# Optimization experiments

Hardware: AMD Instinct MI355X
Metric: run time of the kernel (lower is better)

Reference implementation:

```python
import jax, jax.numpy as jnp
import numpy as np

N_SIDE = 64            # regular RBF kernel grid: 64^3 kernels
LC0_DIM = 32
CMIN, CMAX = -1.0, 1.0
COMBS = [(0, 1), (0, 2), (1, 2)]
# 2^3 cell-corner offsets for the 8 nearest regular-grid kernels
OFFS = np.array([[i, j, k] for i in (0, 1) for j in (0, 1) for k in (0, 1)], dtype=np.int32)


def grid_sample_2d(plane, coords):
    """Bilinear, align_corners=True. plane [C,H,W]; coords [N,2] in [-1,1];
    coords[:,0] indexes W, coords[:,1] indexes H (torch grid_sample convention)."""
    C, H, W = plane.shape
    x = (coords[:, 0] + 1.0) * 0.5 * (W - 1)
    y = (coords[:, 1] + 1.0) * 0.5 * (H - 1)
    x0 = jnp.clip(jnp.floor(x), 0, W - 2).astype(jnp.int32)
    y0 = jnp.clip(jnp.floor(y), 0, H - 2).astype(jnp.int32)
    wx = (x - x0)[None, :]
    wy = (y - y0)[None, :]
    p00 = plane[:, y0, x0]
    p01 = plane[:, y0, x0 + 1]
    p10 = plane[:, y0 + 1, x0]
    p11 = plane[:, y0 + 1, x0 + 1]
    out = p00 * (1 - wx) * (1 - wy) + p01 * wx * (1 - wy) + p10 * (1 - wx) * wy + p11 * wx * wy
    return out.T  # [N,C]


def rbf_features(x, lc0, ks):
    """Regular-grid kNN (8 cell corners) + inverse-quadratic RBF weighting of local codes."""
    interval = (CMAX - CMIN) / (N_SIDE - 1)
    cell = jnp.clip(jnp.floor((x - CMIN) / interval), 0, N_SIDE - 2).astype(jnp.int32)  # [N,3]
    corner = cell[:, None, :] + jnp.asarray(OFFS)[None]                                  # [N,8,3]
    idx = (corner[..., 0] * N_SIDE + corner[..., 1]) * N_SIDE + corner[..., 2]           # [N,8]
    kc = CMIN + corner.astype(x.dtype) * interval                                        # [N,8,3] kernel centers
    d2 = jnp.sum((x[:, None, :] - kc) ** 2, axis=-1)                                     # [N,8]
    s = ks[idx]                                                                          # [N,8] per-kernel shape
    phi = 1.0 / (1.0 + d2 * s * s)                                                       # ivq RBF
    phi = phi / (jnp.sum(phi, axis=-1, keepdims=True) + 1e-8)                            # rbf_lc0_normalize
    codes = lc0[idx]                                                                     # [N,8,LC0_DIM]
    return jnp.einsum('nk,nkd->nd', phi, codes)


def setup_inputs() -> dict:
    key = jax.random.key(0)
    ks_ = jax.random.split(key, 16)
    N = 524288
    aabb = jnp.array([[-1.5, -1.5, -1.5], [1.5, 1.5, 1.5]], dtype=jnp.float32)
    pts = jax.random.uniform(ks_[0], (N, 3), minval=-1.5, maxval=1.5, dtype=jnp.float32)

    def plane(k, r):  # kp_init uniform(0.1, 0.5)
        return jax.random.uniform(k, (32, r, r), minval=0.1, maxval=0.5, dtype=jnp.float32)

    resos = [128, 256, 512]
    inp = {'pts': pts, 'aabb': aabb}
    ki = 1
    for si, r in enumerate(resos):
        for ci in range(3):
            inp[f'p{si}{ci}'] = plane(ks_[ki], r)
            ki += 1
    inp['lc0'] = jax.random.uniform(ks_[ki], (N_SIDE ** 3, LC0_DIM), minval=-1e-4, maxval=1e-4, dtype=jnp.float32)
    interval = (CMAX - CMIN) / (N_SIDE - 1)
    inp['ks'] = jnp.full((N_SIDE ** 3,), 1.0 / interval, dtype=jnp.float32)  # ks_alpha=1.0
    inp['kpb'] = jax.random.uniform(ks_[ki + 1], (96 + LC0_DIM,), minval=-1e-4, maxval=1e-4, dtype=jnp.float32)
    return inp


def reference(pts, aabb, p00, p01, p02, p10, p11, p12, p20, p21, p22, lc0, ks, kpb):
    planes = [[p00, p01, p02], [p10, p11, p12], [p20, p21, p22]]
    # normalize_aabb -> [-1,1]
    x = (pts - aabb[0]) * (2.0 / (aabb[1] - aabb[0])) - 1.0
    # interpolate_ms_features: product over planes within a scale, concat across scales
    feats = []
    for scale in planes:
        interp = 1.0
        for pl, comb in zip(scale, COMBS):
            interp = interp * grid_sample_2d(pl, x[:, list(comb)])
        feats.append(interp)
    kp = jnp.concatenate(feats, axis=-1)          # [N,96]
    rbf = rbf_features(x, lc0, ks)                # [N,32]
    return jnp.concatenate([kp, rbf], axis=-1) + kpb  # [N,128], + kpb bias
```

## Files before the change

### kernel.cpp

```cpp
#include <hip/hip_runtime.h>
#include <hip/hip_bf16.h>
#include <stdint.h>

typedef __hip_bfloat16 bf16;
typedef __hip_bfloat162 bf162;

#define S0 ((size_t)(128*128*32))
#define S1 ((size_t)(256*256*32))
#define S2 ((size_t)(512*512*32))
#define LCN ((size_t)(64*64*64*32))

#define T128 (128*128/64)
#define T256 (256*256/64)
#define T512 (512*512/64)
#define TPLANES (3*T128 + 3*T256 + 3*T512)
#define TLC2 ((int)(LCN/2048))

#define NBUCKETS 32768

__device__ __forceinline__ uint32_t mpart(uint32_t x)
{
    x = (x | (x << 16)) & 0x030000FFu;
    x = (x | (x << 8))  & 0x0300F00Fu;
    x = (x | (x << 4))  & 0x030C30C3u;
    x = (x | (x << 2))  & 0x09249249u;
    return x;
}

__device__ __forceinline__ uint32_t bucket_of(float xn, float yn, float zn)
{
    float bx = fminf(fmaxf(floorf((xn + 1.0f) * 16.0f), 0.0f), 31.0f);
    float by = fminf(fmaxf(floorf((yn + 1.0f) * 16.0f), 0.0f), 31.0f);
    float bz = fminf(fmaxf(floorf((zn + 1.0f) * 16.0f), 0.0f), 31.0f);
    return mpart((uint32_t)bx) | (mpart((uint32_t)by) << 1) | (mpart((uint32_t)bz) << 2);
}

__device__ __forceinline__ uint32_t pack2(float a, float b)
{
    union { bf162 h; uint32_t u; } cv;
    cv.h = __halves2bfloat162(__float2bfloat16(a), __float2bfloat16(b));
    return cv.u;
}

__device__ __forceinline__ void unpack8(uint4 u, float* f)
{
    const bf162* h = (const bf162*)&u;
    f[0] = __bfloat162float(h[0].x); f[1] = __bfloat162float(h[0].y);
    f[2] = __bfloat162float(h[1].x); f[3] = __bfloat162float(h[1].y);
    f[4] = __bfloat162float(h[2].x); f[5] = __bfloat162float(h[2].y);
    f[6] = __bfloat162float(h[3].x); f[7] = __bfloat162float(h[3].y);
}

__global__ __launch_bounds__(256) void zero_counts_kernel(unsigned int* __restrict__ counts)
{
    counts[blockIdx.x * 256 + threadIdx.x] = 0u;
}

__global__ __launch_bounds__(256) void transpose_kernel(
    const float* __restrict__ p00, const float* __restrict__ p01, const float* __restrict__ p02,
    const float* __restrict__ p10, const float* __restrict__ p11, const float* __restrict__ p12,
    const float* __restrict__ p20, const float* __restrict__ p21, const float* __restrict__ p22,
    bf16* __restrict__ tp0, bf16* __restrict__ tp1, bf16* __restrict__ tp2)
{
    const int b = blockIdx.x;
    const int tid = threadIdx.x;
    __shared__ float t[64 * 33];
    const float* src; bf16* dst; int HW, tile;
    if (b < 3 * T128) {
        int pid = b >> 8; tile = b & (T128 - 1); HW = 128 * 128;
        src = pid == 0 ? p00 : (pid == 1 ? p01 : p02);
        dst = tp0 + (size_t)pid * S0;
    } else if (b < 3 * T128 + 3 * T256) {
        int bb = b - 3 * T128; int pid = bb >> 10; tile = bb & (T256 - 1); HW = 256 * 256;
        src = pid == 0 ? p10 : (pid == 1 ? p11 : p12);
        dst = tp1 + (size_t)pid * S1;
    } else {
        int bb = b - 3 * T128 - 3 * T256; int pid = bb >> 12; tile = bb & (T512 - 1); HW = 512 * 512;
        src = pid == 0 ? p20 : (pid == 1 ? p21 : p22);
        dst = tp2 + (size_t)pid * S2;
    }
    const int base = tile * 64;
#pragma unroll
    for (int i = 0; i < 2; ++i) {
        int linear = i * 256 + tid;
        int ch = linear >> 4, pq = linear & 15;
        float4 v = *(const float4*)(src + (size_t)ch * HW + base + pq * 4);
        t[(pq * 4 + 0) * 33 + ch] = v.x;
        t[(pq * 4 + 1) * 33 + ch] = v.y;
        t[(pq * 4 + 2) * 33 + ch] = v.z;
        t[(pq * 4 + 3) * 33 + ch] = v.w;
    }
    __syncthreads();
    {
        int pos = tid >> 2, chunk = tid & 3;
        const float* row = t + pos * 33 + chunk * 8;
        uint4 o;
        o.x = pack2(row[0], row[1]);
        o.y = pack2(row[2], row[3]);
        o.z = pack2(row[4], row[5]);
        o.w = pack2(row[6], row[7]);
        *(uint4*)(dst + (size_t)(base + pos) * 32 + chunk * 8) = o;
    }
}

__global__ __launch_bounds__(256) void lc0cast_kernel(
    const float* __restrict__ lc0, bf16* __restrict__ lc0b)
{
    size_t off = (size_t)blockIdx.x * 2048 + (size_t)threadIdx.x * 8;
    float4 v0 = *(const float4*)(lc0 + off);
    float4 v1 = *(const float4*)(lc0 + off + 4);
    uint4 o;
    o.x = pack2(v0.x, v0.y);
    o.y = pack2(v0.z, v0.w);
    o.z = pack2(v1.x, v1.y);
    o.w = pack2(v1.z, v1.w);
    *(uint4*)(lc0b + off) = o;
}

__global__ __launch_bounds__(256) void hist_kernel(
    const float* __restrict__ pts, const float* __restrict__ aabb,
    unsigned int* __restrict__ counts, int N)
{
    int g = blockIdx.x * 256 + threadIdx.x;
    int b0 = g * 4;
    if (b0 >= N) return;
    float a0 = aabb[0], a1 = aabb[1], a2 = aabb[2];
    float sx = 2.0f / (aabb[3] - a0);
    float sy = 2.0f / (aabb[4] - a1);
    float sz = 2.0f / (aabb[5] - a2);
    if (b0 + 3 < N) {
        const float4* p4 = (const float4*)(pts + (size_t)b0 * 3);
        float4 A = p4[0], B = p4[1], C = p4[2];
        float px[4] = {A.x, A.w, B.z, C.y};
        float py[4] = {A.y, B.x, B.w, C.z};
        float pz[4] = {A.z, B.y, C.x, C.w};
#pragma unroll
        for (int k = 0; k < 4; ++k) {
            float xn = (px[k] - a0) * sx - 1.0f;
            float yn = (py[k] - a1) * sy - 1.0f;
            float zn = (pz[k] - a2) * sz - 1.0f;
            atomicAdd(&counts[bucket_of(xn, yn, zn)], 1u);
        }
    } else {
        for (int i = b0; i < N; ++i) {
            float xn = (pts[3 * (size_t)i + 0] - a0) * sx - 1.0f;
            float yn = (pts[3 * (size_t)i + 1] - a1) * sy - 1.0f;
            float zn = (pts[3 * (size_t)i + 2] - a2) * sz - 1.0f;
            atomicAdd(&counts[bucket_of(xn, yn, zn)], 1u);
        }
    }
}

__global__ __launch_bounds__(1024) void scan_kernel(unsigned int* __restrict__ counts)
{
    __shared__ unsigned int sums[1024];
    const int t = threadIdx.x;
    unsigned int local[32];
    unsigned int s = 0;
#pragma unroll
    for (int i = 0; i < 32; ++i) { local[i] = counts[t * 32 + i]; s += local[i]; }
    sums[t] = s;
    __syncthreads();
    for (int off = 1; off < 1024; off <<= 1) {
        unsigned int v = (t >= off) ? sums[t - off] : 0u;
        __syncthreads();
        sums[t] += v;
        __syncthreads();
    }
    unsigned int run = sums[t] - s;
#pragma unroll
    for (int i = 0; i < 32; ++i) { unsigned int c = local[i]; counts[t * 32 + i] = run; run += c; }
}

__global__ __launch_bounds__(256) void scatter_kernel(
    const float* __restrict__ pts, const float* __restrict__ aabb,
    unsigned int* __restrict__ offsets, float4* __restrict__ sp, int N)
{
    int g = blockIdx.x * 256 + threadIdx.x;
    int b0 = g * 4;
    if (b0 >= N) return;
    float a0 = aabb[0], a1 = aabb[1], a2 = aabb[2];
    float sx = 2.0f / (aabb[3] - a0);
    float sy = 2.0f / (aabb[4] - a1);
    float sz = 2.0f / (aabb[5] - a2);
    if (b0 + 3 < N) {
        const float4* p4 = (const float4*)(pts + (size_t)b0 * 3);
        float4 A = p4[0], B = p4[1], C = p4[2];
        float px[4] = {A.x, A.w, B.z, C.y};
        float py[4] = {A.y, B.x, B.w, C.z};
        float pz[4] = {A.z, B.y, C.x, C.w};
#pragma unroll
        for (int k = 0; k < 4; ++k) {
            float xn = (px[k] - a0) * sx - 1.0f;
            float yn = (py[k] - a1) * sy - 1.0f;
            float zn = (pz[k] - a2) * sz - 1.0f;
            unsigned int pos = atomicAdd(&offsets[bucket_of(xn, yn, zn)], 1u);
            float4 v; v.x = xn; v.y = yn; v.z = zn; v.w = __int_as_float(b0 + k);
            sp[pos] = v;
        }
    } else {
        for (int i = b0; i < N; ++i) {
            float xn = (pts[3 * (size_t)i + 0] - a0) * sx - 1.0f;
            float yn = (pts[3 * (size_t)i + 1] - a1) * sy - 1.0f;
            float zn = (pts[3 * (size_t)i + 2] - a2) * sz - 1.0f;
            unsigned int pos = atomicAdd(&offsets[bucket_of(xn, yn, zn)], 1u);
            float4 v; v.x = xn; v.y = yn; v.z = zn; v.w = __int_as_float(i);
            sp[pos] = v;
        }
    }
}

template <int R>
__device__ __forceinline__ void sample_tp16(const uint4* __restrict__ tq,
                                            float cx, float cy, int cq, float* o)
{
    float gx = (cx + 1.0f) * (0.5f * (float)(R - 1));
    float gy = (cy + 1.0f) * (0.5f * (float)(R - 1));
    float fx = fminf(fmaxf(floorf(gx), 0.0f), (float)(R - 2));
    float fy = fminf(fmaxf(floorf(gy), 0.0f), (float)(R - 2));
    float wx = gx - fx, wy = gy - fy;
    int ix = (int)fx, iy = (int)fy;
    int t00 = (iy * R + ix) * 4 + cq;
    uint4 u00 = tq[t00];
    uint4 u01 = tq[t00 + 4];
    uint4 u10 = tq[t00 + R * 4];
    uint4 u11 = tq[t00 + R * 4 + 4];
    float w11 = wx * wy;
    float w01 = wx - w11;
    float w10 = wy - w11;
    float w00 = 1.0f - wx - wy + w11;
    float a[8], b[8], c[8], d[8];
    unpack8(u00, a); unpack8(u01, b); unpack8(u10, c); unpack8(u11, d);
#pragma unroll
    for (int j = 0; j < 8; ++j)
        o[j] = a[j] * w00 + b[j] * w01 + c[j] * w10 + d[j] * w11;
}

template <int R>
__device__ __forceinline__ void plane_feat16(const uint4* __restrict__ tq,
                                             float xn, float yn, float zn, int cq, float* acc)
{
    const int ps = R * R * 4;
    float t0[8];
    sample_tp16<R>(tq,          xn, yn, cq, acc);
    sample_tp16<R>(tq + ps,     xn, zn, cq, t0);
#pragma unroll
    for (int j = 0; j < 8; ++j) acc[j] *= t0[j];
    sample_tp16<R>(tq + 2 * ps, yn, zn, cq, t0);
#pragma unroll
    for (int j = 0; j < 8; ++j) acc[j] *= t0[j];
}

__device__ __forceinline__ void rbf16(const uint4* __restrict__ lcq,
                                      const float* __restrict__ ks,
                                      float xn, float yn, float zn, int cq, float* acc)
{
    const float interval = 2.0f / 63.0f;
    const float invi = 31.5f;
    float fc0 = fminf(fmaxf(floorf((xn + 1.0f) * invi), 0.0f), 62.0f);
    float fc1 = fminf(fmaxf(floorf((yn + 1.0f) * invi), 0.0f), 62.0f);
    float fc2 = fminf(fmaxf(floorf((zn + 1.0f) * invi), 0.0f), 62.0f);
    int c0 = (int)fc0, c1 = (int)fc1, c2 = (int)fc2;
    float dx0 = xn - (-1.0f + fc0 * interval), dx1 = dx0 - interval;
    float dy0 = yn - (-1.0f + fc1 * interval), dy1 = dy0 - interval;
    float dz0 = zn - (-1.0f + fc2 * interval), dz1 = dz0 - interval;
    int ibase = (c0 * 64 + c1) * 64 + c2;

    float phi[8]; int id[8];
    float sum = 0.0f;
#pragma unroll
    for (int k = 0; k < 8; ++k) {
        int i = (k >> 2) & 1, j = (k >> 1) & 1, l = k & 1;
        int idx = ibase + i * 4096 + j * 64 + l;
        id[k] = idx;
        float ddx = i ? dx1 : dx0;
        float ddy = j ? dy1 : dy0;
        float ddz = l ? dz1 : dz0;
        float dd = ddx * ddx + ddy * ddy + ddz * ddz;
        float s = ks[idx];
        float ph = __builtin_amdgcn_rcpf(fmaf(dd, s * s, 1.0f));
        phi[k] = ph;
        sum += ph;
    }
    float inv = __builtin_amdgcn_rcpf(sum + 1e-8f);
#pragma unroll
    for (int j = 0; j < 8; ++j) acc[j] = 0.0f;
#pragma unroll
    for (int k = 0; k < 8; ++k) {
        float w = phi[k] * inv;
        uint4 u = lcq[id[k] * 4 + cq];
        float v[8]; unpack8(u, v);
#pragma unroll
        for (int j = 0; j < 8; ++j) acc[j] = fmaf(w, v[j], acc[j]);
    }
}

__global__ __launch_bounds__(256) void field16_kernel(
    const uint4* __restrict__ tq0, const uint4* __restrict__ tq1, const uint4* __restrict__ tq2,
    const uint4* __restrict__ lcq,
    const float* __restrict__ ks, const float* __restrict__ kpb,
    const float4* __restrict__ sp, float* __restrict__ out, int N)
{
    const int wave = threadIdx.x >> 6;
    const int lane = threadIdx.x & 63;
    const int p    = lane >> 2;
    const int cq   = lane & 3;
    int bid = blockIdx.x;
    int nb = gridDim.x;
    if ((nb & 7) == 0) bid = (bid & 7) * (nb >> 3) + (bid >> 3);
    const int m = bid * 16 + p;
    if (m >= N) return;

    float4 q = sp[m];
    float xn = q.x, yn = q.y, zn = q.z;
    int n = __float_as_int(q.w);

    float acc[8];
    int base;
    if (wave == 0)      { base = 0;  plane_feat16<128>(tq0, xn, yn, zn, cq, acc); }
    else if (wave == 1) { base = 32; plane_feat16<256>(tq1, xn, yn, zn, cq, acc); }
    else if (wave == 2) { base = 64; plane_feat16<512>(tq2, xn, yn, zn, cq, acc); }
    else                { base = 96; rbf16(lcq, ks, xn, yn, zn, cq, acc); }

    const float* kb = kpb + base + cq * 8;
    float4 k0 = *(const float4*)kb;
    float4 k1 = *(const float4*)(kb + 4);
    float* o = out + (size_t)n * 128 + base + cq * 8;
    float4 r0; r0.x = acc[0] + k0.x; r0.y = acc[1] + k0.y; r0.z = acc[2] + k0.z; r0.w = acc[3] + k0.w;
    float4 r1; r1.x = acc[4] + k1.x; r1.y = acc[5] + k1.y; r1.z = acc[6] + k1.z; r1.w = acc[7] + k1.w;
    *(float4*)o = r0;
    *(float4*)(o + 4) = r1;
}

template <int R>
__device__ __forceinline__ float2 sample_tp(const bf162* __restrict__ tp,
                                            float cx, float cy, int cpair)
{
    float gx = (cx + 1.0f) * (0.5f * (float)(R - 1));
    float gy = (cy + 1.0f) * (0.5f * (float)(R - 1));
    float fx = fminf(fmaxf(floorf(gx), 0.0f), (float)(R - 2));
    float fy = fminf(fmaxf(floorf(gy), 0.0f), (float)(R - 2));
    float wx = gx - fx, wy = gy - fy;
    int ix = (int)fx, iy = (int)fy;
    int i00 = (iy * R + ix) * 16 + cpair;
    int i10 = i00 + R * 16;
    bf162 v00 = tp[i00];
    bf162 v01 = tp[i00 + 16];
    bf162 v10 = tp[i10];
    bf162 v11 = tp[i10 + 16];
    float w11 = wx * wy;
    float w01 = wx - w11;
    float w10 = wy - w11;
    float w00 = 1.0f - wx - wy + w11;
    float2 r;
    r.x = __bfloat162float(v00.x) * w00 + __bfloat162float(v01.x) * w01
        + __bfloat162float(v10.x) * w10 + __bfloat162float(v11.x) * w11;
    r.y = __bfloat162float(v00.y) * w00 + __bfloat162float(v01.y) * w01
        + __bfloat162float(v10.y) * w10 + __bfloat162float(v11.y) * w11;
    return r;
}

template <int R>
__device__ __forceinline__ float2 plane_feat(const bf162* __restrict__ tp,
                                             float xn, float yn, float zn, int cpair)
{
    const int ps = R * R * 16;
    float2 a = sample_tp<R>(tp,          xn, yn, cpair);
    float2 b = sample_tp<R>(tp + ps,     xn, zn, cpair);
    float2 c = sample_tp<R>(tp + 2 * ps, yn, zn, cpair);
    float2 r; r.x = a.x * b.x * c.x; r.y = a.y * b.y * c.y;
    return r;
}

__device__ __forceinline__ float2 sample_f32(const float* __restrict__ pl, int R,
                                             float cx, float cy, int ch)
{
    float gx = (cx + 1.0f) * 0.5f * (float)(R - 1);
    float gy = (cy + 1.0f) * 0.5f * (float)(R - 1);
    float fx = fminf(fmaxf(floorf(gx), 0.0f), (float)(R - 2));
    float fy = fminf(fmaxf(floorf(gy), 0.0f), (float)(R - 2));
    float wx = gx - fx, wy = gy - fy;
    int ix = (int)fx, iy = (int)fy;
    float w11 = wx * wy, w01 = wx - w11, w10 = wy - w11, w00 = 1.0f - wx - wy + w11;
    size_t HW = (size_t)R * R;
    const float* q0 = pl + (size_t)ch * HW + (size_t)iy * R + ix;
    const float* q1 = q0 + HW;
    float2 r;
    r.x = q0[0] * w00 + q0[1] * w01 + q0[R] * w10 + q0[R + 1] * w11;
    r.y = q1[0] * w00 + q1[1] * w01 + q1[R] * w10 + q1[R + 1] * w11;
    return r;
}

template <bool TP>
__device__ __forceinline__ float2 rbf_feat(const bf162* __restrict__ lc0b,
                                           const float* __restrict__ lc0f,
                                           const float* __restrict__ ks,
                                           float xn, float yn, float zn, int cpair)
{
    const float interval = 2.0f / 63.0f;
    const float invi = 31.5f;
    float fc0 = fminf(fmaxf(floorf((xn + 1.0f) * invi), 0.0f), 62.0f);
    float fc1 = fminf(fmaxf(floorf((yn + 1.0f) * invi), 0.0f), 62.0f);
    float fc2 = fminf(fmaxf(floorf((zn + 1.0f) * invi), 0.0f), 62.0f);
    int c0 = (int)fc0, c1 = (int)fc1, c2 = (int)fc2;
    float dx0 = xn - (-1.0f + fc0 * interval), dx1 = dx0 - interval;
    float dy0 = yn - (-1.0f + fc1 * interval), dy1 = dy0 - interval;
    float dz0 = zn - (-1.0f + fc2 * interval), dz1 = dz0 - interval;
    int ibase = (c0 * 64 + c1) * 64 + c2;

    float phi[8]; int id[8];
    float sum = 0.0f;
#pragma unroll
    for (int k = 0; k < 8; ++k) {
        int i = (k >> 2) & 1, j = (k >> 1) & 1, l = k & 1;
        int idx = ibase + i * 4096 + j * 64 + l;
        id[k] = idx;
        float ddx = i ? dx1 : dx0;
        float ddy = j ? dy1 : dy0;
        float ddz = l ? dz1 : dz0;
        float dd = ddx * ddx + ddy * ddy + ddz * ddz;
        float s = ks[idx];
        float ph = __builtin_amdgcn_rcpf(fmaf(dd, s * s, 1.0f));
        phi[k] = ph;
        sum += ph;
    }
    float inv = __builtin_amdgcn_rcpf(sum + 1e-8f);
    float ax = 0.0f, ay = 0.0f;
#pragma unroll
    for (int k = 0; k < 8; ++k) {
        float w = phi[k] * inv;
        float vx, vy;
        if (TP) {
            bf162 v = lc0b[id[k] * 16 + cpair];
            vx = __bfloat162float(v.x); vy = __bfloat162float(v.y);
        } else {
            const float* cp = lc0f + (size_t)id[k] * 32 + 2 * cpair;
            vx = cp[0]; vy = cp[1];
        }
        ax = fmaf(w, vx, ax);
        ay = fmaf(w, vy, ay);
    }
    float2 r; r.x = ax; r.y = ay;
    return r;
}

template <bool TP>
__global__ __launch_bounds__(256) void field_legacy_kernel(
    const float* __restrict__ pts, const float* __restrict__ aabb,
    const float* __restrict__ p00, const float* __restrict__ p01, const float* __restrict__ p02,
    const float* __restrict__ p10, const float* __restrict__ p11, const float* __restrict__ p12,
    const float* __restrict__ p20, const float* __restrict__ p21, const float* __restrict__ p22,
    const bf162* __restrict__ tp0, const bf162* __restrict__ tp1, const bf162* __restrict__ tp2,
    const bf162* __restrict__ lc0b, const float* __restrict__ lc0f,
    const float* __restrict__ ks, const float* __restrict__ kpb,
    float* __restrict__ out, int N)
{
    const int wave  = threadIdx.x >> 6;
    const int lane  = threadIdx.x & 63;
    const int p     = lane >> 4;
    const int cpair = lane & 15;
    const int n = blockIdx.x * 4 + p;
    if (n >= N) return;

    float px = pts[3 * (size_t)n + 0];
    float py = pts[3 * (size_t)n + 1];
    float pz = pts[3 * (size_t)n + 2];
    float xn = (px - aabb[0]) * (2.0f / (aabb[3] - aabb[0])) - 1.0f;
    float yn = (py - aabb[1]) * (2.0f / (aabb[4] - aabb[1])) - 1.0f;
    float zn = (pz - aabb[2]) * (2.0f / (aabb[5] - aabb[2])) - 1.0f;

    float2 val;
    int f;
    if (wave == 0) {
        if (TP) val = plane_feat<128>(tp0, xn, yn, zn, cpair);
        else {
            float2 a = sample_f32(p00, 128, xn, yn, 2 * cpair);
            float2 b = sample_f32(p01, 128, xn, zn, 2 * cpair);
            float2 c = sample_f32(p02, 128, yn, zn, 2 * cpair);
            val.x = a.x * b.x * c.x; val.y = a.y * b.y * c.y;
        }
        f = 2 * cpair;
    } else if (wave == 1) {
        if (TP) val = plane_feat<256>(tp1, xn, yn, zn, cpair);
        else {
            float2 a = sample_f32(p10, 256, xn, yn, 2 * cpair);
            float2 b = sample_f32(p11, 256, xn, zn, 2 * cpair);
            float2 c = sample_f32(p12, 256, yn, zn, 2 * cpair);
            val.x = a.x * b.x * c.x; val.y = a.y * b.y * c.y;
        }
        f = 32 + 2 * cpair;
    } else if (wave == 2) {
        if (TP) val = plane_feat<512>(tp2, xn, yn, zn, cpair);
        else {
            float2 a = sample_f32(p20, 512, xn, yn, 2 * cpair);
            float2 b = sample_f32(p21, 512, xn, zn, 2 * cpair);
            float2 c = sample_f32(p22, 512, yn, zn, 2 * cpair);
            val.x = a.x * b.x * c.x; val.y = a.y * b.y * c.y;
        }
        f = 64 + 2 * cpair;
    } else {
        val = rbf_feat<TP>(lc0b, lc0f, ks, xn, yn, zn, cpair);
        f = 96 + 2 * cpair;
    }

    val.x += kpb[f];
    val.y += kpb[f + 1];
    *(float2*)(out + (size_t)n * 128 + f) = val;
}

extern "C" void kernel_launch(void* const* d_in, const int* in_sizes, int n_in,
                              void* d_out, int out_size, void* d_ws, size_t ws_size,
                              hipStream_t stream)
{
    const float* pts  = (const float*)d_in[0];
    const float* aabb = (const float*)d_in[1];
    const float* pl[9];
    for (int i = 0; i < 9; ++i) pl[i] = (const float*)d_in[2 + i];
    const float* lc0 = (const float*)d_in[11];
    const float* ks  = (const float*)d_in[12];
    const float* kpb = (const float*)d_in[13];
    float* out = (float*)d_out;
    const int N = in_sizes[0] / 3;

    const size_t needTP = (3 * (S0 + S1 + S2) + LCN) * sizeof(bf16);
    const size_t cntOff = needTP;
    const size_t spOff  = cntOff + (size_t)NBUCKETS * 4;
    const size_t needSort = spOff + (size_t)N * 16;

    bf16* w    = (bf16*)d_ws;
    bf16* tp0  = w;
    bf16* tp1  = tp0 + 3 * S0;
    bf16* tp2  = tp1 + 3 * S1;
    bf16* lc0b = tp2 + 3 * S2;
    unsigned int* counts = (unsigned int*)((char*)d_ws + cntOff);
    float4* sp = (float4*)((char*)d_ws + spOff);

    const bool useTP   = (d_ws != nullptr) && (ws_size >= needTP);
    const bool useSort = (d_ws != nullptr) && (ws_size >= needSort);

    if (useSort) {
        const int g4 = (N + 1023) / 1024;
        zero_counts_kernel<<<NBUCKETS / 256, 256, 0, stream>>>(counts);
        hist_kernel<<<g4, 256, 0, stream>>>(pts, aabb, counts, N);
        transpose_kernel<<<TPLANES, 256, 0, stream>>>(
            pl[0], pl[1], pl[2], pl[3], pl[4], pl[5], pl[6], pl[7], pl[8],
            tp0, tp1, tp2);
        lc0cast_kernel<<<TLC2, 256, 0, stream>>>(lc0, lc0b);
        scan_kernel<<<1, 1024, 0, stream>>>(counts);
        scatter_kernel<<<g4, 256, 0, stream>>>(pts, aabb, counts, sp, N);
        const int blocks16 = (N + 15) / 16;
        field16_kernel<<<blocks16, 256, 0, stream>>>(
            (const uint4*)tp0, (const uint4*)tp1, (const uint4*)tp2,
            (const uint4*)lc0b, ks, kpb, sp, out, N);
    } else if (useTP) {
        transpose_kernel<<<TPLANES, 256, 0, stream>>>(
            pl[0], pl[1], pl[2], pl[3], pl[4], pl[5], pl[6], pl[7], pl[8],
            tp0, tp1, tp2);
        lc0cast_kernel<<<TLC2, 256, 0, stream>>>(lc0, lc0b);
        field_legacy_kernel<true><<<(N + 3) / 4, 256, 0, stream>>>(
            pts, aabb, pl[0], pl[1], pl[2], pl[3], pl[4], pl[5], pl[6], pl[7], pl[8],
            (const bf162*)tp0, (const bf162*)tp1, (const bf162*)tp2,
            (const bf162*)lc0b, lc0, ks, kpb, out, N);
    } else {
        field_legacy_kernel<false><<<(N + 3) / 4, 256, 0, stream>>>(
            pts, aabb, pl[0], pl[1], pl[2], pl[3], pl[4], pl[5], pl[6], pl[7], pl[8],
            (const bf162*)d_ws, (const bf162*)d_ws, (const bf162*)d_ws,
            (const bf162*)d_ws, lc0, ks, kpb, out, N);
    }
}
```

Baseline: 587.1 us.

## Merge prep kernels into one launch and batch gather loads before compute

Combines the plane transpose, lc0 bf16 cast and histogram kernels into a single prep_kernel that dispatches on block index, removing two launches and the gaps between them. In the field kernel, all twelve triplane corner loads and all eight RBF code and shape loads are now issued before any arithmetic, so more memory requests are in flight at once. Bilinear interpolation is rewritten with fma chains. Issuing loads together raises register pressure, which could lower occupancy.

New measurement: 577.6 us. About the same (-1.6%).

```diff
diff --git a/kernel.cpp b/kernel.cpp
--- a/kernel.cpp
+++ b/kernel.cpp
@@ -56,70 +56,122 @@
     counts[blockIdx.x * 256 + threadIdx.x] = 0u;
 }
 
-__global__ __launch_bounds__(256) void transpose_kernel(
+__global__ __launch_bounds__(256) void prep_kernel(
     const float* __restrict__ p00, const float* __restrict__ p01, const float* __restrict__ p02,
     const float* __restrict__ p10, const float* __restrict__ p11, const float* __restrict__ p12,
     const float* __restrict__ p20, const float* __restrict__ p21, const float* __restrict__ p22,
-    bf16* __restrict__ tp0, bf16* __restrict__ tp1, bf16* __restrict__ tp2)
+    const float* __restrict__ lc0,
+    bf16* __restrict__ tp0, bf16* __restrict__ tp1, bf16* __restrict__ tp2,
+    bf16* __restrict__ lc0b,
+    const float* __restrict__ pts, const float* __restrict__ aabb,
+    unsigned int* __restrict__ counts, int N)
 {
     const int b = blockIdx.x;
     const int tid = threadIdx.x;
     __shared__ float t[64 * 33];
-    const float* src; bf16* dst; int HW, tile;
-    if (b < 3 * T128) {
-        int pid = b >> 8; tile = b & (T128 - 1); HW = 128 * 128;
-        src = pid == 0 ? p00 : (pid == 1 ? p01 : p02);
-        dst = tp0 + (size_t)pid * S0;
-    } else if (b < 3 * T128 + 3 * T256) {
-        int bb = b - 3 * T128; int pid = bb >> 10; tile = bb & (T256 - 1); HW = 256 * 256;
-        src = pid == 0 ? p10 : (pid == 1 ? p11 : p12);
-        dst = tp1 + (size_t)pid * S1;
+    if (b < TPLANES) {
+        const float* src; bf16* dst; int HW, tile;
+        if (b < 3 * T128) {
+            int pid = b >> 8; tile = b & (T128 - 1); HW = 128 * 128;
+            src = pid == 0 ? p00 : (pid == 1 ? p01 : p02);
+            dst = tp0 + (size_t)pid * S0;
+        } else if (b < 3 * T128 + 3 * T256) {
+            int bb = b - 3 * T128; int pid = bb >> 10; tile = bb & (T256 - 1); HW = 256 * 256;
+            src = pid == 0 ? p10 : (pid == 1 ? p11 : p12);
+            dst = tp1 + (size_t)pid * S1;
+        } else {
+            int bb = b - 3 * T128 - 3 * T256; int pid = bb >> 12; tile = bb & (T512 - 1); HW = 512 * 512;
+            src = pid == 0 ? p20 : (pid == 1 ? p21 : p22);
+            dst = tp2 + (size_t)pid * S2;
+        }
+        const int base = tile * 64;
+#pragma unroll
+        for (int i = 0; i < 2; ++i) {
+            int linear = i * 256 + tid;
+            int ch = linear >> 4, pq = linear & 15;
+            float4 v = *(const float4*)(src + (size_t)ch * HW + base + pq * 4);
+            t[(pq * 4 + 0) * 33 + ch] = v.x;
+            t[(pq * 4 + 1) * 33 + ch] = v.y;
+            t[(pq * 4 + 2) * 33 + ch] = v.z;
+            t[(pq * 4 + 3) * 33 + ch] = v.w;
+        }
+        __syncthreads();
+        {
+            int pos = tid >> 2, chunk = tid & 3;
+            const float* row = t + pos * 33 + chunk * 8;
+            uint4 o;
+            o.x = pack2(row[0], row[1]);
+            o.y = pack2(row[2], row[3]);
+            o.z = pack2(row[4], row[5]);
+            o.w = pack2(row[6], row[7]);
+            *(uint4*)(dst + (size_t)(base + pos) * 32 + chunk * 8) = o;
+        }
+    } else if (b < TPLANES + TLC2) {
+        size_t off = (size_t)(b - TPLANES) * 2048 + (size_t)tid * 8;
+        float4 v0 = *(const float4*)(lc0 + off);
+        float4 v1 = *(const float4*)(lc0 + off + 4);
+        uint4 o;
+        o.x = pack2(v0.x, v0.y);
+        o.y = pack2(v0.z, v0.w);
+        o.z = pack2(v1.x, v1.y);
+        o.w = pack2(v1.z, v1.w);
+        *(uint4*)(lc0b + off) = o;
     } else {
-        int bb = b - 3 * T128 - 3 * T256; int pid = bb >> 12; tile = bb & (T512 - 1); HW = 512 * 512;
-        src = pid == 0 ? p20 : (pid == 1 ? p21 : p22);
-        dst = tp2 + (size_t)pid * S2;
-    }
-    const int base = tile * 64;
-#pragma unroll
-    for (int i = 0; i < 2; ++i) {
-        int linear = i * 256 + tid;
-        int ch = linear >> 4, pq = linear & 15;
-        float4 v = *(const float4*)(src + (size_t)ch * HW + base + pq * 4);
-        t[(pq * 4 + 0) * 33 + ch] = v.x;
-        t[(pq * 4 + 1) * 33 + ch] = v.y;
-        t[(pq * 4 + 2) * 33 + ch] = v.z;
-        t[(pq * 4 + 3) * 33 + ch] = v.w;
-    }
+        int g = (b - TPLANES - TLC2) * 256 + tid;
+        int b0 = g * 4;
+        if (b0 >= N) return;
+        float a0 = aabb[0], a1 = aabb[1], a2 = aabb[2];
+        float sx = 2.0f / (aabb[3] - a0);
+        float sy = 2.0f / (aabb[4] - a1);
+        float sz = 2.0f / (aabb[5] - a2);
+        if (b0 + 3 < N) {
+            const float4* p4 = (const float4*)(pts + (size_t)b0 * 3);
+            float4 A = p4[0], B = p4[1], C = p4[2];
+            float px[4] = {A.x, A.w, B.z, C.y};
+            float py[4] = {A.y, B.x, B.w, C.z};
+            float pz[4] = {A.z, B.y, C.x, C.w};
+#pragma unroll
+            for (int k = 0; k < 4; ++k) {
+                float xn = (px[k] - a0) * sx - 1.0f;
+                float yn = (py[k] - a1) * sy - 1.0f;
+                float zn = (pz[k] - a2) * sz - 1.0f;
+                atomicAdd(&counts[bucket_of(xn, yn, zn)], 1u);
+            }
+        } else {
+            for (int i = b0; i < N; ++i) {
+                float xn = (pts[3 * (size_t)i + 0] - a0) * sx - 1.0f;
+                float yn = (pts[3 * (size_t)i + 1] - a1) * sy - 1.0f;
+                float zn = (pts[3 * (size_t)i + 2] - a2) * sz - 1.0f;
+                atomicAdd(&counts[bucket_of(xn, yn, zn)], 1u);
+            }
+        }
+    }
+}
+
+__global__ __launch_bounds__(1024) void scan_kernel(unsigned int* __restrict__ counts)
+{
+    __shared__ unsigned int sums[1024];
+    const int t = threadIdx.x;
+    unsigned int local[32];
+    unsigned int s = 0;
+#pragma unroll
+    for (int i = 0; i < 32; ++i) { local[i] = counts[t * 32 + i]; s += local[i]; }
+    sums[t] = s;
     __syncthreads();
-    {
-        int pos = tid >> 2, chunk = tid & 3;
-        const float* row = t + pos * 33 + chunk * 8;
-        uint4 o;
-        o.x = pack2(row[0], row[1]);
-        o.y = pack2(row[2], row[3]);
-        o.z = pack2(row[4], row[5]);
-        o.w = pack2(row[6], row[7]);
-        *(uint4*)(dst + (size_t)(base + pos) * 32 + chunk * 8) = o;
-    }
-}
-
-__global__ __launch_bounds__(256) void lc0cast_kernel(
-    const float* __restrict__ lc0, bf16* __restrict__ lc0b)
-{
-    size_t off = (size_t)blockIdx.x * 2048 + (size_t)threadIdx.x * 8;
-    float4 v0 = *(const float4*)(lc0 + off);
-    float4 v1 = *(const float4*)(lc0 + off + 4);
-    uint4 o;
-    o.x = pack2(v0.x, v0.y);
-    o.y = pack2(v0.z, v0.w);
-    o.z = pack2(v1.x, v1.y);
-    o.w = pack2(v1.z, v1.w);
-    *(uint4*)(lc0b + off) = o;
-}
-
-__global__ __launch_bounds__(256) void hist_kernel(
+    for (int off = 1; off < 1024; off <<= 1) {
+        unsigned int v = (t >= off) ? sums[t - off] : 0u;
+        __syncthreads();
+        sums[t] += v;
+        __syncthreads();
+    }
+    unsigned int run = sums[t] - s;
+#pragma unroll
+    for (int i = 0; i < 32; ++i) { unsigned int c = local[i]; counts[t * 32 + i] = run; run += c; }
+}
+
+__global__ __launch_bounds__(256) void scatter_kernel(
     const float* __restrict__ pts, const float* __restrict__ aabb,
-    unsigned int* __restrict__ counts, int N)
+    unsigned int* __restrict__ offsets, float4* __restrict__ sp, int N)
 {
     int g = blockIdx.x * 256 + threadIdx.x;
     int b0 = g * 4;
@@ -139,61 +191,6 @@
             float xn = (px[k] - a0) * sx - 1.0f;
             float yn = (py[k] - a1) * sy - 1.0f;
             float zn = (pz[k] - a2) * sz - 1.0f;
-            atomicAdd(&counts[bucket_of(xn, yn, zn)], 1u);
-        }
-    } else {
-        for (int i = b0; i < N; ++i) {
-            float xn = (pts[3 * (size_t)i + 0] - a0) * sx - 1.0f;
-            float yn = (pts[3 * (size_t)i + 1] - a1) * sy - 1.0f;
-            float zn = (pts[3 * (size_t)i + 2] - a2) * sz - 1.0f;
-            atomicAdd(&counts[bucket_of(xn, yn, zn)], 1u);
-        }
-    }
-}
-
-__global__ __launch_bounds__(1024) void scan_kernel(unsigned int* __restrict__ counts)
-{
-    __shared__ unsigned int sums[1024];
-    const int t = threadIdx.x;
-    unsigned int local[32];
-    unsigned int s = 0;
-#pragma unroll
-    for (int i = 0; i < 32; ++i) { local[i] = counts[t * 32 + i]; s += local[i]; }
-    sums[t] = s;
-    __syncthreads();
-    for (int off = 1; off < 1024; off <<= 1) {
-        unsigned int v = (t >= off) ? sums[t - off] : 0u;
-        __syncthreads();
-        sums[t] += v;
-        __syncthreads();
-    }
-    unsigned int run = sums[t] - s;
-#pragma unroll
-    for (int i = 0; i < 32; ++i) { unsigned int c = local[i]; counts[t * 32 + i] = run; run += c; }
-}
-
-__global__ __launch_bounds__(256) void scatter_kernel(
-    const float* __restrict__ pts, const float* __restrict__ aabb,
-    unsigned int* __restrict__ offsets, float4* __restrict__ sp, int N)
-{
-    int g = blockIdx.x * 256 + threadIdx.x;
-    int b0 = g * 4;
-    if (b0 >= N) return;
-    float a0 = aabb[0], a1 = aabb[1], a2 = aabb[2];
-    float sx = 2.0f / (aabb[3] - a0);
-    float sy = 2.0f / (aabb[4] - a1);
-    float sz = 2.0f / (aabb[5] - a2);
-    if (b0 + 3 < N) {
-        const float4* p4 = (const float4*)(pts + (size_t)b0 * 3);
-        float4 A = p4[0], B = p4[1], C = p4[2];
-        float px[4] = {A.x, A.w, B.z, C.y};
-        float py[4] = {A.y, B.x, B.w, C.z};
-        float pz[4] = {A.z, B.y, C.x, C.w};
-#pragma unroll
-        for (int k = 0; k < 4; ++k) {
-            float xn = (px[k] - a0) * sx - 1.0f;
-            float yn = (py[k] - a1) * sy - 1.0f;
-            float zn = (pz[k] - a2) * sz - 1.0f;
             unsigned int pos = atomicAdd(&offsets[bucket_of(xn, yn, zn)], 1u);
             float4 v; v.x = xn; v.y = yn; v.z = zn; v.w = __int_as_float(b0 + k);
             sp[pos] = v;
@@ -211,8 +208,8 @@
 }
 
 template <int R>
-__device__ __forceinline__ void sample_tp16(const uint4* __restrict__ tq,
-                                            float cx, float cy, int cq, float* o)
+__device__ __forceinline__ void samp_addr(float cx, float cy, int cq,
+                                          int& t00, float4& w)
 {
     float gx = (cx + 1.0f) * (0.5f * (float)(R - 1));
     float gy = (cy + 1.0f) * (0.5f * (float)(R - 1));
@@ -220,20 +217,22 @@
     float fy = fminf(fmaxf(floorf(gy), 0.0f), (float)(R - 2));
     float wx = gx - fx, wy = gy - fy;
     int ix = (int)fx, iy = (int)fy;
-    int t00 = (iy * R + ix) * 4 + cq;
-    uint4 u00 = tq[t00];
-    uint4 u01 = tq[t00 + 4];
-    uint4 u10 = tq[t00 + R * 4];
-    uint4 u11 = tq[t00 + R * 4 + 4];
+    t00 = (iy * R + ix) * 4 + cq;
     float w11 = wx * wy;
-    float w01 = wx - w11;
-    float w10 = wy - w11;
-    float w00 = 1.0f - wx - wy + w11;
+    w.x = 1.0f - wx - wy + w11;
+    w.y = wx - w11;
+    w.z = wy - w11;
+    w.w = w11;
+}
+
+__device__ __forceinline__ void lerp8(uint4 u00, uint4 u01, uint4 u10, uint4 u11,
+                                      float4 w, float* o)
+{
     float a[8], b[8], c[8], d[8];
     unpack8(u00, a); unpack8(u01, b); unpack8(u10, c); unpack8(u11, d);
 #pragma unroll
     for (int j = 0; j < 8; ++j)
-        o[j] = a[j] * w00 + b[j] * w01 + c[j] * w10 + d[j] * w11;
+        o[j] = fmaf(d[j], w.w, fmaf(c[j], w.z, fmaf(b[j], w.y, a[j] * w.x)));
 }
 
 template <int R>
@@ -241,14 +240,25 @@
                                              float xn, float yn, float zn, int cq, float* acc)
 {
     const int ps = R * R * 4;
-    float t0[8];
-    sample_tp16<R>(tq,          xn, yn, cq, acc);
-    sample_tp16<R>(tq + ps,     xn, zn, cq, t0);
-#pragma unroll
-    for (int j = 0; j < 8; ++j) acc[j] *= t0[j];
-    sample_tp16<R>(tq + 2 * ps, yn, zn, cq, t0);
-#pragma unroll
-    for (int j = 0; j < 8; ++j) acc[j] *= t0[j];
+    int tA, tB, tC; float4 wA, wB, wC;
+    samp_addr<R>(xn, yn, cq, tA, wA);
+    samp_addr<R>(xn, zn, cq, tB, wB);
+    samp_addr<R>(yn, zn, cq, tC, wC);
+    const uint4* qA = tq;
+    const uint4* qB = tq + ps;
+    const uint4* qC = tq + 2 * ps;
+    uint4 a00 = qA[tA],         a01 = qA[tA + 4];
+    uint4 a10 = qA[tA + R * 4], a11 = qA[tA + R * 4 + 4];
+    uint4 b00 = qB[tB],         b01 = qB[tB + 4];
+    uint4 b10 = qB[tB + R * 4], b11 = qB[tB + R * 4 + 4];
+    uint4 c00 = qC[tC],         c01 = qC[tC + 4];
+    uint4 c10 = qC[tC + R * 4], c11 = qC[tC + R * 4 + 4];
+    float sA[8], sB[8], sC[8];
+    lerp8(a00, a01, a10, a11, wA, sA);
+    lerp8(b00, b01, b10, b11, wB, sB);
+    lerp8(c00, c01, c10, c11, wC, sC);
+#pragma unroll
+    for (int j = 0; j < 8; ++j) acc[j] = sA[j] * sB[j] * sC[j];
 }
 
 __device__ __forceinline__ void rbf16(const uint4* __restrict__ lcq,
@@ -266,18 +276,30 @@
     float dz0 = zn - (-1.0f + fc2 * interval), dz1 = dz0 - interval;
     int ibase = (c0 * 64 + c1) * 64 + c2;
 
-    float phi[8]; int id[8];
-    float sum = 0.0f;
+    int id[8];
 #pragma unroll
     for (int k = 0; k < 8; ++k) {
         int i = (k >> 2) & 1, j = (k >> 1) & 1, l = k & 1;
-        int idx = ibase + i * 4096 + j * 64 + l;
-        id[k] = idx;
+        id[k] = ibase + i * 4096 + j * 64 + l;
+    }
+    float s0 = ks[id[0]], s1 = ks[id[1]], s2 = ks[id[2]], s3 = ks[id[3]];
+    float s4 = ks[id[4]], s5 = ks[id[5]], s6 = ks[id[6]], s7 = ks[id[7]];
+    uint4 u0 = lcq[id[0] * 4 + cq], u1 = lcq[id[1] * 4 + cq];
+    uint4 u2 = lcq[id[2] * 4 + cq], u3 = lcq[id[3] * 4 + cq];
+    uint4 u4 = lcq[id[4] * 4 + cq], u5 = lcq[id[5] * 4 + cq];
+    uint4 u6 = lcq[id[6] * 4 + cq], u7 = lcq[id[7] * 4 + cq];
+
+    float sarr[8] = {s0, s1, s2, s3, s4, s5, s6, s7};
+    float phi[8];
+    float sum = 0.0f;
+#pragma unroll
+    for (int k = 0; k < 8; ++k) {
+        int i = (k >> 2) & 1, j = (k >> 1) & 1, l = k & 1;
         float ddx = i ? dx1 : dx0;
         float ddy = j ? dy1 : dy0;
         float ddz = l ? dz1 : dz0;
         float dd = ddx * ddx + ddy * ddy + ddz * ddz;
-        float s = ks[idx];
+        float s = sarr[k];
         float ph = __builtin_amdgcn_rcpf(fmaf(dd, s * s, 1.0f));
         phi[k] = ph;
         sum += ph;
@@ -285,11 +307,11 @@
     float inv = __builtin_amdgcn_rcpf(sum + 1e-8f);
 #pragma unroll
     for (int j = 0; j < 8; ++j) acc[j] = 0.0f;
+    uint4 uarr[8] = {u0, u1, u2, u3, u4, u5, u6, u7};
 #pragma unroll
     for (int k = 0; k < 8; ++k) {
         float w = phi[k] * inv;
-        uint4 u = lcq[id[k] * 4 + cq];
-        float v[8]; unpack8(u, v);
+        float v[8]; unpack8(uarr[k], v);
 #pragma unroll
         for (int j = 0; j < 8; ++j) acc[j] = fmaf(w, v[j], acc[j]);
     }
@@ -541,11 +563,9 @@
     if (useSort) {
         const int g4 = (N + 1023) / 1024;
         zero_counts_kernel<<<NBUCKETS / 256, 256, 0, stream>>>(counts);
-        hist_kernel<<<g4, 256, 0, stream>>>(pts, aabb, counts, N);
-        transpose_kernel<<<TPLANES, 256, 0, stream>>>(
+        prep_kernel<<<TPLANES + TLC2 + g4, 256, 0, stream>>>(
             pl[0], pl[1], pl[2], pl[3], pl[4], pl[5], pl[6], pl[7], pl[8],
-            tp0, tp1, tp2);
-        lc0cast_kernel<<<TLC2, 256, 0, stream>>>(lc0, lc0b);
+            lc0, tp0, tp1, tp2, lc0b, pts, aabb, counts, N);
         scan_kernel<<<1, 1024, 0, stream>>>(counts);
         scatter_kernel<<<g4, 256, 0, stream>>>(pts, aabb, counts, sp, N);
         const int blocks16 = (N + 15) / 16;
@@ -553,10 +573,9 @@
             (const uint4*)tp0, (const uint4*)tp1, (const uint4*)tp2,
             (const uint4*)lc0b, ks, kpb, sp, out, N);
     } else if (useTP) {
-        transpose_kernel<<<TPLANES, 256, 0, stream>>>(
+        prep_kernel<<<TPLANES + TLC2, 256, 0, stream>>>(
             pl[0], pl[1], pl[2], pl[3], pl[4], pl[5], pl[6], pl[7], pl[8],
-            tp0, tp1, tp2);
-        lc0cast_kernel<<<TLC2, 256, 0, stream>>>(lc0, lc0b);
+            lc0, tp0, tp1, tp2, lc0b, pts, aabb, nullptr, 0);
         field_legacy_kernel<true><<<(N + 3) / 4, 256, 0, stream>>>(
             pts, aabb, pl[0], pl[1], pl[2], pl[3], pl[4], pl[5], pl[6], pl[7], pl[8],
             (const bf162*)tp0, (const bf162*)tp1, (const bf162*)tp2,
```
